# Kernel optimization log

Hardware: AMD Instinct MI355X
Metric: run time of the kernel (lower is better)

## Reference

```python
import jax, jax.numpy as jnp
import numpy as np

N, E = 40000, 640000
IN_DIM, EDGE_DIM, HID, H1 = 5, 11, 128, 4
NEG_SLOPE = 0.2


def _add_self_loops(ei, ea, n):
    # PyG GATConv default: add_self_loops=True, fill_value='mean' for edge_attr
    loop = jnp.arange(n, dtype=ei.dtype)
    ei2 = jnp.concatenate([ei, jnp.stack([loop, loop])], axis=1)
    ea2 = jnp.concatenate([ea, jnp.broadcast_to(ea.mean(0), (n, ea.shape[1]))], axis=0)
    return ei2, ea2


def _gat(x, ei, ea, W, We, a_src, a_dst, a_edge, b, H, C):
    # Single GATConv layer (eval mode, dropout inactive)
    n = x.shape[0]
    xh = (x @ W).reshape(n, H, C)            # [N,H,C]
    eh = (ea @ We).reshape(-1, H, C)         # [E,H,C]
    src, dst = ei[0], ei[1]
    a_s = (xh * a_src).sum(-1)               # [N,H]
    a_d = (xh * a_dst).sum(-1)               # [N,H]
    alpha = jax.nn.leaky_relu(a_s[src] + a_d[dst] + (eh * a_edge).sum(-1), NEG_SLOPE)  # [E,H]
    amax = jax.ops.segment_max(alpha, dst, num_segments=n)
    ex = jnp.exp(alpha - amax[dst])
    den = jax.ops.segment_sum(ex, dst, num_segments=n)
    w = ex / (den[dst] + 1e-16)              # softmax over inbound edges per dst
    out = jax.ops.segment_sum(xh[src] * w[:, :, None], dst, num_segments=n)  # [N,H,C]
    return out.reshape(n, H * C) + b


def setup_inputs() -> dict:
    key = jax.random.key(0)
    ks = jax.random.split(key, 20)
    s = 0.1
    return {
        "x": jax.random.normal(ks[0], (N, IN_DIM), jnp.float32),
        "edge_index": jax.random.randint(ks[1], (2, E), 0, N),
        "edge_attr": jax.random.normal(ks[2], (E, EDGE_DIM), jnp.float32),
        "W1": jax.random.normal(ks[3], (IN_DIM, H1 * HID), jnp.float32) * s,
        "We1": jax.random.normal(ks[4], (EDGE_DIM, H1 * HID), jnp.float32) * s,
        "a_src1": jax.random.normal(ks[5], (H1, HID), jnp.float32) * s,
        "a_dst1": jax.random.normal(ks[6], (H1, HID), jnp.float32) * s,
        "a_edge1": jax.random.normal(ks[7], (H1, HID), jnp.float32) * s,
        "b1": jnp.zeros((H1 * HID,), jnp.float32),
        # layer 2 (512 -> 128, 1 head)
        "W2": jax.random.normal(ks[8], (H1 * HID, HID), jnp.float32) * s,
        "We2": jax.random.normal(ks[9], (EDGE_DIM, HID), jnp.float32) * s,
        "a_src2": jax.random.normal(ks[10], (1, HID), jnp.float32) * s,
        "a_dst2": jax.random.normal(ks[11], (1, HID), jnp.float32) * s,
        "a_edge2": jax.random.normal(ks[12], (1, HID), jnp.float32) * s,
        "b2": jnp.zeros((HID,), jnp.float32),
        # final linear 128 -> 1
        "Wfc": jax.random.normal(ks[13], (HID, 1), jnp.float32) * s,
        "bfc": jnp.zeros((1,), jnp.float32),
    }


def reference(x, edge_index, edge_attr,
              W1, We1, a_src1, a_dst1, a_edge1, b1,
              W2, We2, a_src2, a_dst2, a_edge2, b2,
              Wfc, bfc):
    ei, ea = _add_self_loops(edge_index, edge_attr, x.shape[0])
    h = jax.nn.relu(_gat(x, ei, ea, W1, We1, a_src1, a_dst1, a_edge1, b1, H1, HID))
    h = jax.nn.relu(_gat(h, ei, ea, W2, We2, a_src2, a_dst2, a_edge2, b2, 1, HID))
    return jax.nn.sigmoid(h @ Wfc + bfc)
```

## Files before the change

kernel.cpp:

```cpp
#include <hip/hip_runtime.h>

#define NN   40000
#define EE   640000
#define EE2  680000
#define IND  5
#define ED   11
#define HIDD 128
#define F1   512

typedef unsigned short u16;
typedef unsigned int   u32;
typedef __attribute__((ext_vector_type(8))) short bf16x8;
typedef __attribute__((ext_vector_type(4))) float f32x4;

__device__ __forceinline__ float bf2f(u16 u) { return __uint_as_float(((u32)u) << 16); }
__device__ __forceinline__ u16 f2bf(float f) {
    u32 u = __float_as_uint(f);
    return (u16)((u + 0x7FFFu + ((u >> 16) & 1u)) >> 16);
}

__device__ __forceinline__ float wsum(float v) {
#pragma unroll
    for (int o = 32; o; o >>= 1) v += __shfl_xor(v, o, 64);
    return v;
}
__device__ __forceinline__ float lrelu(float v) { return v > 0.f ? v : 0.2f * v; }


__global__ void k_init(float* __restrict__ consts, int* __restrict__ counts) {
    int i = blockIdx.x * blockDim.x + threadIdx.x;
    if (i < 256) consts[i] = 0.f;
    if (i < NN) counts[i] = 0;
}

__global__ void k_constsA(float* __restrict__ consts,
                          const float* __restrict__ We1, const float* __restrict__ ae1,
                          const float* __restrict__ We2, const float* __restrict__ ae2) {
    int t = threadIdx.x;
    if (t < 44) {
        int k = t >> 2, h = t & 3;
        float s = 0.f;
        for (int c = 0; c < HIDD; ++c)
            s += We1[k * F1 + h * HIDD + c] * ae1[h * HIDD + c];
        consts[16 + t] = s;
    }
    if (t >= 48 && t < 48 + ED) {
        int k = t - 48;
        float s = 0.f;
        for (int c = 0; c < HIDD; ++c)
            s += We2[k * HIDD + c] * ae2[c];
        consts[64 + k] = s;
    }
}

__global__ void k_constsB(float* __restrict__ consts) {
    int t = threadIdx.x;
    if (t < ED) consts[t] *= (1.0f / (float)EE);
    __syncthreads();
    if (t < 4) {
        float s = 0.f;
        for (int k = 0; k < ED; ++k) s += consts[k] * consts[16 + k * 4 + t];
        consts[80 + t] = s;
    }
    if (t == 8) {
        float s = 0.f;
        for (int k = 0; k < ED; ++k) s += consts[k] * consts[64 + k];
        consts[96] = s;
    }
}

__global__ void k_wswz(const float* __restrict__ W2,
                       u16* __restrict__ bhi, u16* __restrict__ blo) {
    int t = blockIdx.x * blockDim.x + threadIdx.x;
    if (t >= 8192) return;
    int lane = t & 63, ks = (t >> 6) & 15, nt = t >> 10;
    int kbase = ks * 32 + (lane >> 4) * 8;
    int n = nt * 16 + (lane & 15);
    size_t dst = (size_t)t * 8;
#pragma unroll
    for (int j = 0; j < 8; ++j) {
        float v = W2[(size_t)(kbase + j) * HIDD + n];
        u16 h = f2bf(v);
        float resid = v - bf2f(h);
        bhi[dst + j] = h;
        blo[dst + j] = f2bf(resid);
    }
}

__global__ void k_count(const int* __restrict__ ei, int* __restrict__ counts,
                        int* __restrict__ rank) {
    int i = blockIdx.x * blockDim.x + threadIdx.x;
    if (i >= EE) return;
    rank[i] = atomicAdd(&counts[ei[EE + i]], 1);
}

#define SBLK 256
#define SGRID ((NN + SBLK - 1) / SBLK)
__global__ void __launch_bounds__(SBLK) k_scanA(const int* __restrict__ counts,
                                                int* __restrict__ local_ex,
                                                int* __restrict__ bsum) {
    __shared__ int sh[SBLK];
    int t = threadIdx.x;
    int i = blockIdx.x * SBLK + t;
    int v = (i < NN) ? counts[i] + 1 : 0;
    sh[t] = v;
    __syncthreads();
    for (int o = 1; o < SBLK; o <<= 1) {
        int u = (t >= o) ? sh[t - o] : 0;
        __syncthreads();
        sh[t] += u;
        __syncthreads();
    }
    if (i < NN) local_ex[i] = sh[t] - v;
    if (t == SBLK - 1) bsum[blockIdx.x] = sh[t];
}

__global__ void __launch_bounds__(SBLK) k_scanB(int* __restrict__ bsum,
                                                int* __restrict__ boff) {
    __shared__ int sh[SBLK];
    int t = threadIdx.x;
    int v = (t < SGRID) ? bsum[t] : 0;
    sh[t] = v;
    __syncthreads();
    for (int o = 1; o < SBLK; o <<= 1) {
        int u = (t >= o) ? sh[t - o] : 0;
        __syncthreads();
        sh[t] += u;
        __syncthreads();
    }
    if (t < SGRID) boff[t] = sh[t] - v;
}

__global__ void __launch_bounds__(SBLK) k_scanC(const int* __restrict__ local_ex,
                                                const int* __restrict__ boff,
                                                int* __restrict__ row_off) {
    int t = threadIdx.x;
    int i = blockIdx.x * SBLK + t;
    if (i < NN) row_off[i] = local_ex[i] + boff[blockIdx.x];
    if (i == 0) row_off[NN] = EE2;
}

__global__ void __launch_bounds__(256) k_build(const float* __restrict__ ea,
                                               const int* __restrict__ ei,
                                               const int* __restrict__ rank,
                                               const int* __restrict__ row_off,
                                               float* consts,
                                               uint4* __restrict__ rec) {
    int i = blockIdx.x * 256 + threadIdx.x;
    int s = ei[i];
    int d = ei[EE + i];
    int pos = row_off[d] + rank[i];
    const float* row = ea + (size_t)i * ED;
    float r[ED];
#pragma unroll
    for (int k = 0; k < ED; ++k) r[k] = row[k];
    float e0 = 0.f, e1 = 0.f, e2 = 0.f, e3 = 0.f, et = 0.f;
#pragma unroll
    for (int k = 0; k < ED; ++k) {
        float a = r[k];
        e0 += a * consts[16 + k * 4 + 0];
        e1 += a * consts[16 + k * 4 + 1];
        e2 += a * consts[16 + k * 4 + 2];
        e3 += a * consts[16 + k * 4 + 3];
        et += a * consts[64 + k];
    }
    uint4 q;
    q.x = (u32)f2bf(e0) | ((u32)f2bf(e1) << 16);
    q.y = (u32)f2bf(e2) | ((u32)f2bf(e3) << 16);
    q.z = (u32)s;
    q.w = __float_as_uint(et);
    rec[pos] = q;
    __shared__ float ls[4 * ED];
#pragma unroll
    for (int k = 0; k < ED; ++k) r[k] = wsum(r[k]);
    int wv = threadIdx.x >> 6;
    if ((threadIdx.x & 63) == 0) {
#pragma unroll
        for (int k = 0; k < ED; ++k) ls[wv * ED + k] = r[k];
    }
    __syncthreads();
    int tt = threadIdx.x;
    if (tt < ED)
        atomicAdd(&consts[tt], ls[tt] + ls[ED + tt] + ls[2 * ED + tt] + ls[3 * ED + tt]);
}

__global__ void k_self(const int* __restrict__ row_off, const int* __restrict__ counts,
                       const float* __restrict__ consts, uint4* __restrict__ rec) {
    int n = blockIdx.x * blockDim.x + threadIdx.x;
    if (n >= NN) return;
    int pos = row_off[n] + counts[n];
    uint4 q;
    q.x = (u32)f2bf(consts[80]) | ((u32)f2bf(consts[81]) << 16);
    q.y = (u32)f2bf(consts[82]) | ((u32)f2bf(consts[83]) << 16);
    q.z = (u32)n;
    q.w = __float_as_uint(consts[96]);
    rec[pos] = q;
}

__global__ void __launch_bounds__(64) k_xh1(const float* __restrict__ x,
                                            const float* __restrict__ W1,
                                            const float* __restrict__ as1,
                                            const float* __restrict__ ad1,
                                            float* __restrict__ aS1,
                                            float* __restrict__ aD1) {
    int n = blockIdx.x, t = threadIdx.x;
    int c0 = t * 8, h = t >> 4;
    const float* xp = x + (size_t)n * IND;
    float x0 = xp[0], x1 = xp[1], x2 = xp[2], x3 = xp[3], x4 = xp[4];
    float p = 0.f, q = 0.f;
#pragma unroll
    for (int j = 0; j < 8; ++j) {
        int c = c0 + j;
        float v = x0 * W1[0 * F1 + c] + x1 * W1[1 * F1 + c] + x2 * W1[2 * F1 + c]
                + x3 * W1[3 * F1 + c] + x4 * W1[4 * F1 + c];
        p += v * as1[c];
        q += v * ad1[c];
    }
#pragma unroll
    for (int o = 1; o <= 8; o <<= 1) {
        p += __shfl_xor(p, o, 64);
        q += __shfl_xor(q, o, 64);
    }
    if ((t & 15) == 0) {
        aS1[n * 4 + h] = p;
        aD1[n * 4 + h] = q;
    }
}

__global__ void __launch_bounds__(64) k_agg1(const int* __restrict__ row_off,
                                             const uint4* __restrict__ rec,
                                             const float* __restrict__ aS1,
                                             const float* __restrict__ aD1,
                                             const float* __restrict__ x,
                                             const float* __restrict__ W1,
                                             const float* __restrict__ b1,
                                             u16* __restrict__ h1) {
    int n = blockIdx.x, t = threadIdx.x;
    int s0 = row_off[n], s1 = row_off[n + 1];
    int h = t & 3;
    float4 adv = *(const float4*)(aD1 + (size_t)n * 4);
    float adh = (h == 0) ? adv.x : (h == 1) ? adv.y : (h == 2) ? adv.z : adv.w;
    float z = 0.f, xa0 = 0.f, xa1 = 0.f, xa2 = 0.f, xa3 = 0.f, xa4 = 0.f;
    for (int i = s0 + (t >> 2); i < s1; i += 16) {
        uint4 q = rec[i];
        u32 w2 = (h & 2) ? q.y : q.x;
        float eh = bf2f((h & 1) ? (u16)(w2 >> 16) : (u16)(w2 & 0xFFFF));
        int s = (int)q.z;
        float a = lrelu(eh + aS1[(size_t)s * 4 + h] + adh);
        float ex = __expf(a);
        z += ex;
        const float* xp = x + (size_t)s * IND;
        xa0 += ex * xp[0]; xa1 += ex * xp[1]; xa2 += ex * xp[2];
        xa3 += ex * xp[3]; xa4 += ex * xp[4];
    }
#pragma unroll
    for (int o = 4; o <= 32; o <<= 1) {
        z   += __shfl_xor(z, o, 64);
        xa0 += __shfl_xor(xa0, o, 64); xa1 += __shfl_xor(xa1, o, 64);
        xa2 += __shfl_xor(xa2, o, 64); xa3 += __shfl_xor(xa3, o, 64);
        xa4 += __shfl_xor(xa4, o, 64);
    }
    int ho = t >> 4;
    float zz = __shfl(z, ho);
    float y0 = __shfl(xa0, ho), y1 = __shfl(xa1, ho), y2 = __shfl(xa2, ho);
    float y3 = __shfl(xa3, ho), y4 = __shfl(xa4, ho);
    float ih = 1.f / (zz + 1e-16f);
    int c0 = t * 8;
#pragma unroll
    for (int j = 0; j < 8; ++j) {
        int c = c0 + j;
        float v = (y0 * W1[0 * F1 + c] + y1 * W1[1 * F1 + c] + y2 * W1[2 * F1 + c]
                 + y3 * W1[3 * F1 + c] + y4 * W1[4 * F1 + c]) * ih;
        h1[(size_t)n * F1 + c] = f2bf(fmaxf(v + b1[c], 0.f));
    }
}

__global__ void __launch_bounds__(256, 2) k_gemm2(const u16* __restrict__ h1,
                                                  const u16* __restrict__ bhi,
                                                  const u16* __restrict__ blo,
                                                  const float* __restrict__ as2,
                                                  const float* __restrict__ ad2,
                                                  u16* __restrict__ xh2,
                                                  float* __restrict__ aS2,
                                                  float* __restrict__ aD2) {
    int tid = threadIdx.x;
    int wv = tid >> 6, lane = tid & 63;
    int tile = blockIdx.x * 4 + wv;
    if (tile >= 2500) return;
    int n0 = tile * 16;
    int mrow = lane & 15, quad = lane >> 4;
    const u16* aptr = h1 + (size_t)(n0 + mrow) * F1 + quad * 8;
    const u16* bbase_hi = bhi + lane * 8;
    const u16* bbase_lo = blo + lane * 8;
    f32x4 acc[8];
#pragma unroll
    for (int nt = 0; nt < 8; ++nt) acc[nt] = (f32x4){0.f, 0.f, 0.f, 0.f};

    bf16x8 bh0[8], bl0[8], bh1[8], bl1[8];
    bf16x8 af0, af1;
    af0 = *(const bf16x8*)(aptr);
#pragma unroll
    for (int nt = 0; nt < 8; ++nt) {
        bh0[nt] = *(const bf16x8*)(bbase_hi + nt * 8192);
        bl0[nt] = *(const bf16x8*)(bbase_lo + nt * 8192);
    }
#pragma unroll
    for (int ks = 0; ks < 16; ++ks) {
        if (ks < 15) {
            af1 = *(const bf16x8*)(aptr + (ks + 1) * 32);
#pragma unroll
            for (int nt = 0; nt < 8; ++nt) {
                bh1[nt] = *(const bf16x8*)(bbase_hi + nt * 8192 + (ks + 1) * 512);
                bl1[nt] = *(const bf16x8*)(bbase_lo + nt * 8192 + (ks + 1) * 512);
            }
        }
#pragma unroll
        for (int nt = 0; nt < 8; ++nt) {
            acc[nt] = __builtin_amdgcn_mfma_f32_16x16x32_bf16(af0, bh0[nt], acc[nt], 0, 0, 0);
            acc[nt] = __builtin_amdgcn_mfma_f32_16x16x32_bf16(af0, bl0[nt], acc[nt], 0, 0, 0);
        }
        af0 = af1;
#pragma unroll
        for (int nt = 0; nt < 8; ++nt) { bh0[nt] = bh1[nt]; bl0[nt] = bl1[nt]; }
    }
    float ps[4] = {0.f, 0.f, 0.f, 0.f}, pd[4] = {0.f, 0.f, 0.f, 0.f};
#pragma unroll
    for (int nt = 0; nt < 8; ++nt) {
        int col = nt * 16 + mrow;
        float sa = as2[col], da = ad2[col];
#pragma unroll
        for (int r = 0; r < 4; ++r) {
            float v = acc[nt][r];
            xh2[(size_t)(n0 + quad * 4 + r) * HIDD + col] = f2bf(v);
            ps[r] += v * sa; pd[r] += v * da;
        }
    }
#pragma unroll
    for (int r = 0; r < 4; ++r) {
#pragma unroll
        for (int o = 1; o <= 8; o <<= 1) {
            ps[r] += __shfl_xor(ps[r], o, 64);
            pd[r] += __shfl_xor(pd[r], o, 64);
        }
        if (mrow == 0) {
            aS2[n0 + quad * 4 + r] = ps[r];
            aD2[n0 + quad * 4 + r] = pd[r];
        }
    }
}

__global__ void __launch_bounds__(64) k_agg2(const int* __restrict__ row_off,
                                             const uint4* __restrict__ rec,
                                             const float* __restrict__ aS2,
                                             const float* __restrict__ aD2,
                                             const u16* __restrict__ xh2,
                                             const float* __restrict__ bias2,
                                             const float* __restrict__ Wfc,
                                             const float* __restrict__ bfc,
                                             float* __restrict__ out) {
    int n = blockIdx.x, t = threadIdx.x;
    int s0 = row_off[n], s1 = row_off[n + 1];
    float adn = aD2[n];
    int g = t >> 4, l = t & 15;
    int c0 = l * 8;
    float z = 0.f;
    float acc[8];
#pragma unroll
    for (int j = 0; j < 8; ++j) acc[j] = 0.f;
    for (int i = s0 + g; i < s1; i += 4) {
        uint4 qe = rec[i];
        int s = (int)qe.z;
        float et2 = __uint_as_float(qe.w);
        float ex = __expf(lrelu(aS2[s] + adn + et2));
        z += ex;
        uint4 q = *(const uint4*)(xh2 + (size_t)s * HIDD + c0);
        acc[0] += ex * bf2f((u16)(q.x & 0xFFFF)); acc[1] += ex * bf2f((u16)(q.x >> 16));
        acc[2] += ex * bf2f((u16)(q.y & 0xFFFF)); acc[3] += ex * bf2f((u16)(q.y >> 16));
        acc[4] += ex * bf2f((u16)(q.z & 0xFFFF)); acc[5] += ex * bf2f((u16)(q.z >> 16));
        acc[6] += ex * bf2f((u16)(q.w & 0xFFFF)); acc[7] += ex * bf2f((u16)(q.w >> 16));
    }
#pragma unroll
    for (int o = 16; o <= 32; o <<= 1) {
        z += __shfl_xor(z, o, 64);
#pragma unroll
        for (int j = 0; j < 8; ++j) acc[j] += __shfl_xor(acc[j], o, 64);
    }
    float inv = 1.f / (z + 1e-16f);
    float p = 0.f;
#pragma unroll
    for (int j = 0; j < 8; ++j) {
        float o = fmaxf(acc[j] * inv + bias2[c0 + j], 0.f);
        p += o * Wfc[c0 + j];
    }
#pragma unroll
    for (int o = 1; o <= 8; o <<= 1) p += __shfl_xor(p, o, 64);
    if (t == 0) {
        float logit = p + bfc[0];
        out[n] = 1.f / (1.f + __expf(-logit));
    }
}

extern "C" void kernel_launch(void* const* d_in, const int* in_sizes, int n_in,
                              void* d_out, int out_size, void* d_ws, size_t ws_size,
                              hipStream_t stream) {
    (void)in_sizes; (void)n_in; (void)out_size; (void)ws_size;
    const float* x   = (const float*)d_in[0];
    const int*   ei  = (const int*)d_in[1];
    const float* ea  = (const float*)d_in[2];
    const float* W1  = (const float*)d_in[3];
    const float* We1 = (const float*)d_in[4];
    const float* as1 = (const float*)d_in[5];
    const float* ad1 = (const float*)d_in[6];
    const float* ae1 = (const float*)d_in[7];
    const float* b1  = (const float*)d_in[8];
    const float* W2  = (const float*)d_in[9];
    const float* We2 = (const float*)d_in[10];
    const float* as2 = (const float*)d_in[11];
    const float* ad2 = (const float*)d_in[12];
    const float* ae2 = (const float*)d_in[13];
    const float* b2v = (const float*)d_in[14];
    const float* Wfc = (const float*)d_in[15];
    const float* bfc = (const float*)d_in[16];
    float* out = (float*)d_out;

    char* ws = (char*)d_ws;
    size_t off = 0;
    auto take = [&](size_t nb) {
        size_t r = off;
        off += (nb + 255) & ~(size_t)255;
        return r;
    };
    float* consts = (float*)(ws + take(1024));
    int* row_off  = (int*)(ws + take((size_t)(NN + 1) * 4));
    int* counts   = (int*)(ws + take((size_t)NN * 4));
    int* local_ex = (int*)(ws + take((size_t)NN * 4));
    int* bsum     = (int*)(ws + take(1024));
    int* boff     = (int*)(ws + take(1024));
    int* rank     = (int*)(ws + take((size_t)EE * 4));
    uint4* rec    = (uint4*)(ws + take((size_t)EE2 * 16));
    float* aS1    = (float*)(ws + take((size_t)NN * 16));
    float* aD1    = (float*)(ws + take((size_t)NN * 16));
    float* aS2    = (float*)(ws + take((size_t)NN * 4));
    float* aD2    = (float*)(ws + take((size_t)NN * 4));
    u16* h1       = (u16*)(ws + take((size_t)NN * F1 * 2));
    u16* xh2      = (u16*)(ws + take((size_t)NN * HIDD * 2));
    u16* w2hi     = (u16*)(ws + take((size_t)65536 * 2));
    u16* w2lo     = (u16*)(ws + take((size_t)65536 * 2));

    k_init<<<(NN + 255) / 256, 256, 0, stream>>>(consts, counts);
    k_constsA<<<1, 64, 0, stream>>>(consts, We1, ae1, We2, ae2);
    k_wswz<<<32, 256, 0, stream>>>(W2, w2hi, w2lo);
    k_count<<<(EE + 255) / 256, 256, 0, stream>>>(ei, counts, rank);
    k_scanA<<<SGRID, SBLK, 0, stream>>>(counts, local_ex, bsum);
    k_scanB<<<1, SBLK, 0, stream>>>(bsum, boff);
    k_scanC<<<SGRID, SBLK, 0, stream>>>(local_ex, boff, row_off);

    k_build<<<EE / 256, 256, 0, stream>>>(ea, ei, rank, row_off, consts, rec);
    k_constsB<<<1, 64, 0, stream>>>(consts);
    k_self<<<(NN + 255) / 256, 256, 0, stream>>>(row_off, counts, consts, rec);

    k_xh1<<<NN, 64, 0, stream>>>(x, W1, as1, ad1, aS1, aD1);
    k_agg1<<<NN, 64, 0, stream>>>(row_off, rec, aS1, aD1, x, W1, b1, h1);

    k_gemm2<<<625, 256, 0, stream>>>(h1, w2hi, w2lo, as2, ad2, xh2, aS2, aD2);
    k_agg2<<<NN, 64, 0, stream>>>(row_off, rec, aS2, aD2, xh2, b2v, Wfc, bfc, out);
}
```

Baseline: 288.5 us.

## Pack four nodes per block and replace edge-attr atomics with a deterministic reduction

The per-node kernels (xh1, agg1, agg2) now run four 64-thread wavefronts per 256-thread block, one node per wavefront, so the launch has a quarter as many blocks. The edge-attribute mean no longer uses atomicAdd into consts. Each wavefront writes its partial sums to a buffer, and a new single-block kernel reduces them and applies the 1/E scale. This removes atomic contention and makes the mean deterministic, at the cost of an extra launch and a serial single-block reduction over 10000 partials.

```diff
diff --git a/kernel.cpp b/kernel.cpp
--- a/kernel.cpp
+++ b/kernel.cpp
@@ -7,6 +7,7 @@
 #define ED   11
 #define HIDD 128
 #define F1   512
+#define NBW  10000
 
 typedef unsigned short u16;
 typedef unsigned int   u32;
@@ -55,7 +56,6 @@
 
 __global__ void k_constsB(float* __restrict__ consts) {
     int t = threadIdx.x;
-    if (t < ED) consts[t] *= (1.0f / (float)EE);
     __syncthreads();
     if (t < 4) {
         float s = 0.f;
@@ -144,8 +144,9 @@
                                                const int* __restrict__ ei,
                                                const int* __restrict__ rank,
                                                const int* __restrict__ row_off,
-                                               float* consts,
-                                               uint4* __restrict__ rec) {
+                                               const float* __restrict__ consts,
+                                               uint4* __restrict__ rec,
+                                               float* __restrict__ psum) {
     int i = blockIdx.x * 256 + threadIdx.x;
     int s = ei[i];
     int d = ei[EE + i];
@@ -170,18 +171,35 @@
     q.z = (u32)s;
     q.w = __float_as_uint(et);
     rec[pos] = q;
-    __shared__ float ls[4 * ED];
 #pragma unroll
     for (int k = 0; k < ED; ++k) r[k] = wsum(r[k]);
-    int wv = threadIdx.x >> 6;
-    if ((threadIdx.x & 63) == 0) {
-#pragma unroll
-        for (int k = 0; k < ED; ++k) ls[wv * ED + k] = r[k];
-    }
-    __syncthreads();
-    int tt = threadIdx.x;
-    if (tt < ED)
-        atomicAdd(&consts[tt], ls[tt] + ls[ED + tt] + ls[2 * ED + tt] + ls[3 * ED + tt]);
+    int wgid = blockIdx.x * 4 + (threadIdx.x >> 6);
+    int lane = threadIdx.x & 63;
+    if (lane < ED) psum[wgid * ED + lane] = r[lane];
+}
+
+__global__ void __launch_bounds__(256) k_sumred(const float* __restrict__ psum,
+                                                float* __restrict__ consts) {
+    __shared__ float sh[256 * 4];
+    int t = threadIdx.x;
+    float acc[ED];
+#pragma unroll
+    for (int k = 0; k < ED; ++k) acc[k] = 0.f;
+    for (int w = t; w < NBW; w += 256) {
+        const float* p = psum + (size_t)w * ED;
+#pragma unroll
+        for (int k = 0; k < ED; ++k) acc[k] += p[k];
+    }
+    for (int k = 0; k < ED; ++k) {
+        sh[t] = acc[k];
+        __syncthreads();
+        for (int o = 128; o; o >>= 1) {
+            if (t < o) sh[t] += sh[t + o];
+            __syncthreads();
+        }
+        if (t == 0) consts[k] = sh[0] * (1.0f / (float)EE);
+        __syncthreads();
+    }
 }
 
 __global__ void k_self(const int* __restrict__ row_off, const int* __restrict__ counts,
@@ -197,13 +215,14 @@
     rec[pos] = q;
 }
 
-__global__ void __launch_bounds__(64) k_xh1(const float* __restrict__ x,
-                                            const float* __restrict__ W1,
-                                            const float* __restrict__ as1,
-                                            const float* __restrict__ ad1,
-                                            float* __restrict__ aS1,
-                                            float* __restrict__ aD1) {
-    int n = blockIdx.x, t = threadIdx.x;
+__global__ void __launch_bounds__(256) k_xh1(const float* __restrict__ x,
+                                             const float* __restrict__ W1,
+                                             const float* __restrict__ as1,
+                                             const float* __restrict__ ad1,
+                                             float* __restrict__ aS1,
+                                             float* __restrict__ aD1) {
+    int n = blockIdx.x * 4 + (threadIdx.x >> 6);
+    int t = threadIdx.x & 63;
     int c0 = t * 8, h = t >> 4;
     const float* xp = x + (size_t)n * IND;
     float x0 = xp[0], x1 = xp[1], x2 = xp[2], x3 = xp[3], x4 = xp[4];
@@ -227,15 +246,16 @@
     }
 }
 
-__global__ void __launch_bounds__(64) k_agg1(const int* __restrict__ row_off,
-                                             const uint4* __restrict__ rec,
-                                             const float* __restrict__ aS1,
-                                             const float* __restrict__ aD1,
-                                             const float* __restrict__ x,
-                                             const float* __restrict__ W1,
-                                             const float* __restrict__ b1,
-                                             u16* __restrict__ h1) {
-    int n = blockIdx.x, t = threadIdx.x;
+__global__ void __launch_bounds__(256) k_agg1(const int* __restrict__ row_off,
+                                              const uint4* __restrict__ rec,
+                                              const float* __restrict__ aS1,
+                                              const float* __restrict__ aD1,
+                                              const float* __restrict__ x,
+                                              const float* __restrict__ W1,
+                                              const float* __restrict__ b1,
+                                              u16* __restrict__ h1) {
+    int n = blockIdx.x * 4 + (threadIdx.x >> 6);
+    int t = threadIdx.x & 63;
     int s0 = row_off[n], s1 = row_off[n + 1];
     int h = t & 3;
     float4 adv = *(const float4*)(aD1 + (size_t)n * 4);
@@ -349,16 +369,17 @@
     }
 }
 
-__global__ void __launch_bounds__(64) k_agg2(const int* __restrict__ row_off,
-                                             const uint4* __restrict__ rec,
-                                             const float* __restrict__ aS2,
-                                             const float* __restrict__ aD2,
-                                             const u16* __restrict__ xh2,
-                                             const float* __restrict__ bias2,
-                                             const float* __restrict__ Wfc,
-                                             const float* __restrict__ bfc,
-                                             float* __restrict__ out) {
-    int n = blockIdx.x, t = threadIdx.x;
+__global__ void __launch_bounds__(256) k_agg2(const int* __restrict__ row_off,
+                                              const uint4* __restrict__ rec,
+                                              const float* __restrict__ aS2,
+                                              const float* __restrict__ aD2,
+                                              const u16* __restrict__ xh2,
+                                              const float* __restrict__ bias2,
+                                              const float* __restrict__ Wfc,
+                                              const float* __restrict__ bfc,
+                                              float* __restrict__ out) {
+    int n = blockIdx.x * 4 + (threadIdx.x >> 6);
+    int t = threadIdx.x & 63;
     int s0 = row_off[n], s1 = row_off[n + 1];
     float adn = aD2[n];
     int g = t >> 4, l = t & 15;
@@ -437,6 +458,7 @@
     int* bsum     = (int*)(ws + take(1024));
     int* boff     = (int*)(ws + take(1024));
     int* rank     = (int*)(ws + take((size_t)EE * 4));
+    float* psum   = (float*)(ws + take((size_t)NBW * ED * 4));
     uint4* rec    = (uint4*)(ws + take((size_t)EE2 * 16));
     float* aS1    = (float*)(ws + take((size_t)NN * 16));
     float* aD1    = (float*)(ws + take((size_t)NN * 16));
@@ -455,13 +477,14 @@
     k_scanB<<<1, SBLK, 0, stream>>>(bsum, boff);
     k_scanC<<<SGRID, SBLK, 0, stream>>>(local_ex, boff, row_off);
 
-    k_build<<<EE / 256, 256, 0, stream>>>(ea, ei, rank, row_off, consts, rec);
+    k_build<<<EE / 256, 256, 0, stream>>>(ea, ei, rank, row_off, consts, rec, psum);
+    k_sumred<<<1, 256, 0, stream>>>(psum, consts);
     k_constsB<<<1, 64, 0, stream>>>(consts);
     k_self<<<(NN + 255) / 256, 256, 0, stream>>>(row_off, counts, consts, rec);
 
-    k_xh1<<<NN, 64, 0, stream>>>(x, W1, as1, ad1, aS1, aD1);
-    k_agg1<<<NN, 64, 0, stream>>>(row_off, rec, aS1, aD1, x, W1, b1, h1);
+    k_xh1<<<NN / 4, 256, 0, stream>>>(x, W1, as1, ad1, aS1, aD1);
+    k_agg1<<<NN / 4, 256, 0, stream>>>(row_off, rec, aS1, aD1, x, W1, b1, h1);
 
     k_gemm2<<<625, 256, 0, stream>>>(h1, w2hi, w2lo, as2, ad2, xh2, aS2, aD2);
-    k_agg2<<<NN, 64, 0, stream>>>(row_off, rec, aS2, aD2, xh2, b2v, Wfc, bfc, out);
-}
+    k_agg2<<<NN / 4, 256, 0, stream>>>(row_off, rec, aS2, aD2, xh2, b2v, Wfc, bfc, out);
+}
```

After: 296.7 us. +2.8%, slower.
